# Performance work log

Measured on AMD Instinct MI355X. Metric: run time of the kernel, lower is better.

## Reference

```python
import jax, jax.numpy as jnp
import numpy as np
import math

B, N, C, H = 4, 4096, 1024, 4
D = C // H            # per-head channel dim = 256
KV_SIZE = 1024        # config.KV_sizec, used as the score scale
EPS = 1e-5            # InstanceNorm2d default eps


def setup_inputs() -> dict:
    key = jax.random.key(0)
    ks = jax.random.split(key, 9)
    f = lambda k, shape: jax.random.normal(k, shape, dtype=jnp.float32) * 0.05
    return {
        'S':   f(ks[0], (B, N, C)),
        'SKV': f(ks[1], (B, N, C)),
        'T':   f(ks[2], (B, N, C)),
        'TKV': f(ks[3], (B, N, C)),
        'Wq':  f(ks[4], (H, D, D)),   # per-head torch Linear weights [out,in]
        'Wk':  f(ks[5], (H, D, D)),
        'Wv':  f(ks[6], (H, D, D)),
        'Wout':  f(ks[7], (C, C)),
        'Woutd': f(ks[8], (C, C)),
    }


def _heads(x, W):
    # x: [B,N,C] split into H chunks of D along channels; per-head Linear (no bias).
    xh = x.reshape(B, N, H, D)
    return jnp.einsum('bnhd,hed->bhne', xh, W)  # [B,H,N,D]


def _inorm(s):
    # InstanceNorm2d (affine=False): normalize over the last two dims per (batch, head).
    m = jnp.mean(s, axis=(-2, -1), keepdims=True)
    v = jnp.var(s, axis=(-2, -1), keepdims=True)
    return (s - m) * jax.lax.rsqrt(v + EPS)


def _attend(Q, K, V, Wout):
    # Channel attention: scores [B,H,D,D], sequence dim contracted.
    scores = jnp.einsum('bhni,bhnj->bhij', Q, K) / math.sqrt(KV_SIZE)
    probs = jax.nn.softmax(_inorm(scores), axis=-1)
    ctx = jnp.einsum('bhij,bhnj->bhin', probs, V)          # [B,H,D,N]
    # permute(0,3,2,1) -> [B,N,D,H], then view merges (D,H) with head fastest.
    ctx = jnp.transpose(ctx, (0, 3, 2, 1)).reshape(B, N, C)
    return jnp.einsum('bnc,oc->bno', ctx, Wout)


def reference(S, SKV, T, TKV, Wq, Wk, Wv, Wout, Woutd):
    Q  = _heads(S,   Wq); K  = _heads(SKV, Wk); V  = _heads(SKV, Wv)
    Qd = _heads(T,   Wq); Kd = _heads(TKV, Wk); Vd = _heads(TKV, Wv)
    S2T   = _attend(Q,  Kd, Vd, Wout)   # cross: S queries, T keys/values
    T2S   = _attend(Qd, K,  V,  Woutd)  # cross: T queries, S keys/values
    S_out = _attend(Q,  K,  V,  Wout)   # self on S
    T_out = _attend(Qd, Kd, Vd, Woutd)  # self on T
    return (S_out, T2S, S2T, T_out)
```

## Files before the change

### kernel.cpp

```cpp
#include <hip/hip_runtime.h>
#include <hip/hip_bf16.h>
#include <cstdint>

using bf16 = __hip_bfloat16;
typedef __attribute__((ext_vector_type(8))) short bf16x8v;
typedef __attribute__((ext_vector_type(4))) float f32x4v;

__device__ __forceinline__ void gload_lds16(const void* g, void* l) {
  __builtin_amdgcn_global_load_lds(
      (const __attribute__((address_space(1))) void*)g,
      (__attribute__((address_space(3))) void*)l, 16, 0, 0);
}

__device__ __forceinline__ unsigned short f2bu(float x) {
  union { __hip_bfloat16 h; unsigned short u; } cv;
  cv.h = __float2bfloat16(x);
  return cv.u;
}

__device__ __forceinline__ bf16x8v cvt8(const f32x4v lo, const f32x4v hi) {
  bf16x8v t;
  t[0] = (short)f2bu(lo[0]); t[1] = (short)f2bu(lo[1]);
  t[2] = (short)f2bu(lo[2]); t[3] = (short)f2bu(lo[3]);
  t[4] = (short)f2bu(hi[0]); t[5] = (short)f2bu(hi[1]);
  t[6] = (short)f2bu(hi[2]); t[7] = (short)f2bu(hi[3]);
  return t;
}

struct GemmP {
  const void* A; const void* B; const void* A2; const void* B2; void* C;
  int K, lda, ldb, ldc, tilesN, swz;
  int d0, d1, d2;
  long long sA0, sA1, sA2, sA3;
  long long sB0, sB1, sB2, sB3;
  long long sC0, sC1, sC2, sC3;
  long long zA, zB, zC;
  float scale;
};

template<int OUT_F32, int AF32, int BF32>
__global__ __launch_bounds__(256, 4)
void gemm_bt(GemmP p)
{
  constexpr int EA = AF32 ? 4 : 2;
  constexpr int EB = BF32 ? 4 : 2;
  constexpr int ABYTES = 128 * 64 * EA;
  constexpr int BBYTES = 128 * 64 * EB;
  constexpr int SEGA = ABYTES / 4096;
  constexpr int SEGB = BBYTES / 4096;
  __shared__ __attribute__((aligned(1024))) char smem[ABYTES + BBYTES];
  const int tid  = threadIdx.x;
  const int lane = tid & 63;
  const int wid  = tid >> 6;

  int bx = blockIdx.x;
  if (p.swz) {
    const int nx = gridDim.x;
    const int q = nx >> 3, r = nx & 7;
    const int xcd = bx & 7, loc = bx >> 3;
    bx = (xcd < r ? xcd * (q + 1) : r * (q + 1) + (xcd - r) * q) + loc;
  }
  const int tn = bx % p.tilesN;
  const int tm = bx / p.tilesN;
  int idx = blockIdx.y;
  const int i0 = idx % p.d0; idx /= p.d0;
  const int i1 = idx % p.d1; idx /= p.d1;
  const int i2 = idx % p.d2;
  const int i3 = idx / p.d2;

  const char* Abase = (const char*)((p.A2 && i2) ? p.A2 : p.A);
  const char* Bbase = (const char*)((p.B2 && i2) ? p.B2 : p.B);
  const long long offA = (long long)i0*p.sA0 + (long long)i1*p.sA1 +
                         (long long)i2*p.sA2 + (long long)i3*p.sA3 +
                         (long long)blockIdx.z*p.zA;
  const long long offB = (long long)i0*p.sB0 + (long long)i1*p.sB1 +
                         (long long)i2*p.sB2 + (long long)i3*p.sB3 +
                         (long long)blockIdx.z*p.zB;
  const char* Am = Abase + offA * EA;
  const char* Bm = Bbase + offB * EB;
  const int bm = tm * 128, bn = tn * 128;

  const char* asrc[SEGA]; int aseg[SEGA];
  #pragma unroll
  for (int r = 0; r < SEGA; ++r) {
    const int oseg = (wid * SEGA + r) * 1024;
    const int o = oseg + lane * 16;
    int row, srcoff;
    if constexpr (AF32) { row = o >> 8; const int s = (o >> 4) & 15; srcoff = (s ^ (row & 15)) * 4; }
    else               { row = o >> 7; const int s = (o >> 4) & 7;  srcoff = (s ^ (row & 7)) * 8;  }
    aseg[r] = oseg;
    asrc[r] = Am + ((long long)(bm + row) * p.lda + srcoff) * EA;
  }
  const char* bsrc[SEGB]; int bseg[SEGB];
  #pragma unroll
  for (int r = 0; r < SEGB; ++r) {
    const int oseg = (wid * SEGB + r) * 1024;
    const int o = oseg + lane * 16;
    int row, srcoff;
    if constexpr (BF32) { row = o >> 8; const int s = (o >> 4) & 15; srcoff = (s ^ (row & 15)) * 4; }
    else               { row = o >> 7; const int s = (o >> 4) & 7;  srcoff = (s ^ (row & 7)) * 8;  }
    bseg[r] = oseg;
    bsrc[r] = Bm + ((long long)(bn + row) * p.ldb + srcoff) * EB;
  }

  f32x4v acc[4][4];
  #pragma unroll
  for (int i = 0; i < 4; ++i)
    #pragma unroll
    for (int j = 0; j < 4; ++j) acc[i][j] = (f32x4v){0.f, 0.f, 0.f, 0.f};

  const int wr = wid >> 1, wc = wid & 1;
  const int fr_a = wr * 64 + (lane & 15);
  const int fr_b = wc * 64 + (lane & 15);
  const int fch  = lane >> 4;

  const int nK = p.K / 64;
  for (int kt = 0; kt < nK; ++kt) {
    #pragma unroll
    for (int r = 0; r < SEGA; ++r) { gload_lds16(asrc[r], smem + aseg[r]); asrc[r] += 64 * EA; }
    #pragma unroll
    for (int r = 0; r < SEGB; ++r) { gload_lds16(bsrc[r], smem + ABYTES + bseg[r]); bsrc[r] += 64 * EB; }
    __syncthreads();
    #pragma unroll
    for (int kk = 0; kk < 2; ++kk) {
      bf16x8v a[4], b[4];
      #pragma unroll
      for (int mi = 0; mi < 4; ++mi) {
        const int row = fr_a + mi * 16;
        if constexpr (AF32) {
          const int c2 = (fch + kk * 4) * 2;
          const f32x4v lo = *(const f32x4v*)(smem + row * 256 + ((c2 ^ (row & 15)) << 4));
          const f32x4v hi = *(const f32x4v*)(smem + row * 256 + (((c2 + 1) ^ (row & 15)) << 4));
          a[mi] = cvt8(lo, hi);
        } else {
          a[mi] = *(const bf16x8v*)(smem + row * 128 + (((fch + kk * 4) ^ (row & 7)) << 4));
        }
      }
      #pragma unroll
      for (int ni = 0; ni < 4; ++ni) {
        const int row = fr_b + ni * 16;
        if constexpr (BF32) {
          const int c2 = (fch + kk * 4) * 2;
          const f32x4v lo = *(const f32x4v*)(smem + ABYTES + row * 256 + ((c2 ^ (row & 15)) << 4));
          const f32x4v hi = *(const f32x4v*)(smem + ABYTES + row * 256 + (((c2 + 1) ^ (row & 15)) << 4));
          b[ni] = cvt8(lo, hi);
        } else {
          b[ni] = *(const bf16x8v*)(smem + ABYTES + row * 128 + (((fch + kk * 4) ^ (row & 7)) << 4));
        }
      }
      #pragma unroll
      for (int mi = 0; mi < 4; ++mi)
        #pragma unroll
        for (int ni = 0; ni < 4; ++ni)
          acc[mi][ni] = __builtin_amdgcn_mfma_f32_16x16x32_bf16(a[mi], b[ni], acc[mi][ni], 0, 0, 0);
    }
    __syncthreads();
  }

  const long long coff = (long long)i0*p.sC0 + (long long)i1*p.sC1 +
                         (long long)i2*p.sC2 + (long long)i3*p.sC3 +
                         (long long)blockIdx.z*p.zC;
  const int col0 = bn + wc * 64 + (lane & 15);
  const int row0 = bm + wr * 64 + ((lane >> 4) << 2);
  if (OUT_F32) {
    float* Cp = (float*)p.C + coff;
    #pragma unroll
    for (int mi = 0; mi < 4; ++mi)
      #pragma unroll
      for (int ni = 0; ni < 4; ++ni)
        #pragma unroll
        for (int j = 0; j < 4; ++j)
          Cp[(size_t)(row0 + mi*16 + j) * p.ldc + (col0 + ni*16)] = acc[mi][ni][j] * p.scale;
  } else {
    bf16* Cp = (bf16*)p.C + coff;
    #pragma unroll
    for (int mi = 0; mi < 4; ++mi)
      #pragma unroll
      for (int ni = 0; ni < 4; ++ni)
        #pragma unroll
        for (int j = 0; j < 4; ++j)
          Cp[(size_t)(row0 + mi*16 + j) * p.ldc + (col0 + ni*16)] =
              __float2bfloat16(acc[mi][ni][j] * p.scale);
  }
}

struct KVP {
  const float* X0; const float* X1;
  const bf16* Wk; const bf16* Wv;
  bf16* KT; bf16* Vc;
};

__global__ __launch_bounds__(256, 2)
void kv_fused(KVP p)
{
  __shared__ __attribute__((aligned(1024))) char smem[65536];
  const int tid = threadIdx.x, lane = tid & 63, wid = tid >> 6;
  const int jt = blockIdx.x & 1, nt = blockIdx.x >> 1;
  int idx = blockIdx.y;
  const int h = idx & 3; idx >>= 2;
  const int b = idx & 3; idx >>= 2;
  const int vi = idx;
  const float* X = (vi ? p.X1 : p.X0) + (size_t)b * 4194304 + (size_t)h * 256;
  const bf16* Wk = p.Wk + (size_t)h * 65536;
  const bf16* Wv = p.Wv + (size_t)h * 65536;
  const int n0 = nt * 128, j0 = jt * 128;

  const float* xsrc[8];
  #pragma unroll
  for (int r = 0; r < 8; ++r) {
    const int o = (wid * 8 + r) * 1024 + lane * 16;
    const int row = o >> 8, s = (o >> 4) & 15;
    xsrc[r] = X + (size_t)(n0 + row) * 1024 + (s ^ (row & 15)) * 4;
  }
  const bf16 *wksrc[4], *wvsrc[4];
  #pragma unroll
  for (int r = 0; r < 4; ++r) {
    const int o = (wid * 4 + r) * 1024 + lane * 16;
    const int row = o >> 7, s = (o >> 4) & 7;
    wksrc[r] = Wk + (size_t)(j0 + row) * 256 + (s ^ (row & 7)) * 8;
    wvsrc[r] = Wv + (size_t)(j0 + row) * 256 + (s ^ (row & 7)) * 8;
  }

  f32x4v accK[4][4], accV[4][4];
  #pragma unroll
  for (int i = 0; i < 4; ++i)
    #pragma unroll
    for (int j = 0; j < 4; ++j) {
      accK[i][j] = (f32x4v){0.f, 0.f, 0.f, 0.f};
      accV[i][j] = (f32x4v){0.f, 0.f, 0.f, 0.f};
    }

  const int wr = wid >> 1, wc = wid & 1;
  const int frW = wr * 64 + (lane & 15);
  const int frX = wc * 64 + (lane & 15);
  const int fch = lane >> 4;

  for (int kt = 0; kt < 4; ++kt) {
    #pragma unroll
    for (int r = 0; r < 8; ++r) { gload_lds16(xsrc[r], smem + (wid * 8 + r) * 1024); xsrc[r] += 64; }
    #pragma unroll
    for (int r = 0; r < 4; ++r) {
      gload_lds16(wksrc[r], smem + 32768 + (wid * 4 + r) * 1024); wksrc[r] += 64;
      gload_lds16(wvsrc[r], smem + 49152 + (wid * 4 + r) * 1024); wvsrc[r] += 64;
    }
    __syncthreads();
    #pragma unroll
    for (int kk = 0; kk < 2; ++kk) {
      bf16x8v wk[4], wv[4], x[4];
      #pragma unroll
      for (int mi = 0; mi < 4; ++mi) {
        const int row = frW + mi * 16;
        const int byo = row * 128 + (((fch + kk * 4) ^ (row & 7)) << 4);
        wk[mi] = *(const bf16x8v*)(smem + 32768 + byo);
        wv[mi] = *(const bf16x8v*)(smem + 49152 + byo);
      }
      #pragma unroll
      for (int ni = 0; ni < 4; ++ni) {
        const int row = frX + ni * 16;
        const int c2 = (fch + kk * 4) * 2;
        const f32x4v lo = *(const f32x4v*)(smem + row * 256 + ((c2 ^ (row & 15)) << 4));
        const f32x4v hi = *(const f32x4v*)(smem + row * 256 + (((c2 + 1) ^ (row & 15)) << 4));
        x[ni] = cvt8(lo, hi);
      }
      #pragma unroll
      for (int mi = 0; mi < 4; ++mi)
        #pragma unroll
        for (int ni = 0; ni < 4; ++ni) {
          accK[mi][ni] = __builtin_amdgcn_mfma_f32_16x16x32_bf16(wk[mi], x[ni], accK[mi][ni], 0, 0, 0);
          accV[ni][mi] = __builtin_amdgcn_mfma_f32_16x16x32_bf16(x[ni], wv[mi], accV[ni][mi], 0, 0, 0);
        }
    }
    __syncthreads();
  }

  const size_t kbase = (size_t)vi * 16777216 + (size_t)b * 4194304 + (size_t)h * 1048576;
  const size_t vbase = (size_t)vi * 16777216 + (size_t)b * 4194304;
  bf16* Kp = p.KT + kbase;
  bf16* Vp = p.Vc + vbase;
  const int rW = ((lane >> 4) << 2);
  #pragma unroll
  for (int mi = 0; mi < 4; ++mi)
    #pragma unroll
    for (int ni = 0; ni < 4; ++ni)
      #pragma unroll
      for (int j = 0; j < 4; ++j) {
        const int jrow = j0 + wr * 64 + mi * 16 + rW + j;
        const int ncol = n0 + wc * 64 + ni * 16 + (lane & 15);
        Kp[(size_t)jrow * 4096 + ncol] = __float2bfloat16(accK[mi][ni][j]);
        const int nrow = n0 + wc * 64 + ni * 16 + rW + j;
        const int jcol = j0 + wr * 64 + mi * 16 + (lane & 15);
        Vp[(size_t)nrow * 1024 + h * 256 + jcol] = __float2bfloat16(accV[ni][mi][j]);
      }
}

__global__ void cvt3_f32_bf16(const float* __restrict__ a0, const float* __restrict__ a1,
                              const float* __restrict__ a2,
                              unsigned short* __restrict__ out, long long ostride, int n4) {
  const int i = blockIdx.x * 256 + threadIdx.x;
  if (i >= n4) return;
  const float* src = (blockIdx.y == 0) ? a0 : (blockIdx.y == 1) ? a1 : a2;
  const float4 v = ((const float4*)src)[i];
  ushort4 o;
  o.x = f2bu(v.x); o.y = f2bu(v.y); o.z = f2bu(v.z); o.w = f2bu(v.w);
  ((ushort4*)(out + (size_t)blockIdx.y * ostride))[i] = o;
}

__global__ void wpre_kernel(const float* __restrict__ Wout, const float* __restrict__ Woutd,
                            bf16* __restrict__ Wpre) {
  const int w = blockIdx.y;
  const int flat = blockIdx.x * 256 + threadIdx.x;
  const float* Wsrc = w ? Woutd : Wout;
  const int o  = flat >> 10;
  const int c2 = flat & 1023;
  const int h  = c2 >> 8;
  const int i  = c2 & 255;
  Wpre[(size_t)w * 1048576 + flat] = __float2bfloat16(Wsrc[o * 1024 + i * 4 + h]);
}

__global__ __launch_bounds__(256)
void stats_quarter(const float* __restrict__ sp, float* __restrict__ st) {
  const int m = blockIdx.x >> 2, q = blockIdx.x & 3;
  const size_t PS = 4194304;
  const float* s = sp + (size_t)m * 65536 + (size_t)q * 16384;
  const int tid = threadIdx.x, lane = tid & 63, w = tid >> 6;

  float sum = 0.f, sq = 0.f;
  for (int i = tid; i < 4096; i += 256) {
    const float4 a = ((const float4*)s)[i];
    const float4 b = ((const float4*)(s + PS))[i];
    const float4 c = ((const float4*)(s + 2 * PS))[i];
    const float4 d = ((const float4*)(s + 3 * PS))[i];
    const float x0 = (a.x + b.x) + (c.x + d.x);
    const float x1 = (a.y + b.y) + (c.y + d.y);
    const float x2 = (a.z + b.z) + (c.z + d.z);
    const float x3 = (a.w + b.w) + (c.w + d.w);
    sum += (x0 + x1) + (x2 + x3);
    sq  += (x0 * x0 + x1 * x1) + (x2 * x2 + x3 * x3);
  }
  #pragma unroll
  for (int o = 32; o; o >>= 1) { sum += __shfl_xor(sum, o); sq += __shfl_xor(sq, o); }
  __shared__ float red[8];
  if (lane == 0) { red[w] = sum; red[4 + w] = sq; }
  __syncthreads();
  if (tid == 0) {
    st[blockIdx.x * 2]     = (red[0] + red[1]) + (red[2] + red[3]);
    st[blockIdx.x * 2 + 1] = (red[4] + red[5]) + (red[6] + red[7]);
  }
}

__global__ __launch_bounds__(256)
void softmax_t(const float* __restrict__ sp, const float* __restrict__ st,
               bf16* __restrict__ pr) {
  const int m = blockIdx.x >> 2, iq = blockIdx.x & 3;
  const size_t PS = 4194304;
  const float sum = (st[m*8+0] + st[m*8+2]) + (st[m*8+4] + st[m*8+6]);
  const float sq  = (st[m*8+1] + st[m*8+3]) + (st[m*8+5] + st[m*8+7]);
  const float mean = sum * (1.f / 65536.f);
  const float var  = sq * (1.f / 65536.f) - mean * mean;
  const float inv  = rsqrtf(var + 1e-5f);

  const int tid = threadIdx.x;
  const int i  = iq * 64 + (tid & 63);
  const int jq = tid >> 6;
  const float* cb = sp + (size_t)m * 65536 + i;

  float e[64];
  float se = 0.f;
  #pragma unroll
  for (int jj = 0; jj < 64; ++jj) {
    const size_t o = (size_t)(jq * 64 + jj) * 256;
    const float v = (cb[o] + cb[PS + o]) + (cb[2 * PS + o] + cb[3 * PS + o]);
    e[jj] = __expf((v - mean) * inv);
    se += e[jj];
  }
  __shared__ float seb[256];
  seb[tid] = se;
  __syncthreads();
  const int c = tid & 63;
  const float rvs = 1.f / ((seb[c] + seb[c + 64]) + (seb[c + 128] + seb[c + 192]));
  bf16* pc = pr + (size_t)m * 65536 + i;
  #pragma unroll
  for (int jj = 0; jj < 64; ++jj)
    pc[(size_t)(jq * 64 + jj) * 256] = __float2bfloat16(e[jj] * rvs);
}

extern "C" void kernel_launch(void* const* d_in, const int* in_sizes, int n_in,
                              void* d_out, int out_size, void* d_ws, size_t ws_size,
                              hipStream_t stream)
{
  const float* S     = (const float*)d_in[0];
  const float* SKV   = (const float*)d_in[1];
  const float* T     = (const float*)d_in[2];
  const float* TKV   = (const float*)d_in[3];
  const float* Wq    = (const float*)d_in[4];
  const float* Wk    = (const float*)d_in[5];
  const float* Wv    = (const float*)d_in[6];
  const float* Wout  = (const float*)d_in[7];
  const float* Woutd = (const float*)d_in[8];
  float* out = (float*)d_out;

  const int Hd = 4, Dd = 256;
  const long long NC  = 4096ll * 1024;
  const long long BNC = 4 * NC;
  const long long HDN = 1048576;

  char* ws = (char*)d_ws;
  size_t off = 0;
  auto alloc = [&](size_t bytes) -> void* {
    void* pp = ws + off; off += (bytes + 255) & ~(size_t)255; return pp;
  };
  bf16*  Wqb    = (bf16*)alloc((size_t)Hd * Dd * Dd * 2);
  bf16*  Wkb    = (bf16*)alloc((size_t)Hd * Dd * Dd * 2);
  bf16*  Wvb    = (bf16*)alloc((size_t)Hd * Dd * Dd * 2);
  bf16*  Wpre   = (bf16*)alloc(2ull * 1024 * 1024 * 2);
  bf16*  QT     = (bf16*)alloc(2 * BNC * 2);
  bf16*  KT     = (bf16*)alloc(2 * BNC * 2);
  bf16*  Vc     = (bf16*)alloc(2 * BNC * 2);
  float* sparts = (float*)alloc(4ull * 4194304 * 4);
  float* stats  = (float*)alloc(256ull * 2 * 4);
  bf16*  probsT = (bf16*)alloc(64ull * 65536 * 2);
  bf16*  Weff   = QT;
  if (ws_size < off) return;

  {
    const int w4 = (Hd * Dd * Dd) / 4;
    cvt3_f32_bf16<<<dim3((w4 + 255) / 256, 3), dim3(256), 0, stream>>>(
        Wq, Wk, Wv, (unsigned short*)Wqb, (long long)Hd * Dd * Dd, w4);
    wpre_kernel<<<dim3(4096, 2), dim3(256), 0, stream>>>(Wout, Woutd, Wpre);
  }

  GemmP g{};

  g.A = Wqb; g.B = S; g.A2 = nullptr; g.B2 = T; g.C = QT;
  g.K = 256; g.lda = 256; g.ldb = 1024; g.ldc = 4096; g.tilesN = 32; g.swz = 0;
  g.d0 = 4; g.d1 = 4; g.d2 = 2;
  g.sA0 = 65536; g.sA1 = 0;  g.sA2 = 0;   g.sA3 = 0;
  g.sB0 = 256;   g.sB1 = NC; g.sB2 = 0;   g.sB3 = 0;
  g.sC0 = HDN;   g.sC1 = NC; g.sC2 = BNC; g.sC3 = 0;
  g.zA = 0; g.zB = 0; g.zC = 0;
  g.scale = 1.f;
  gemm_bt<0, 0, 1><<<dim3(2 * 32, 32), dim3(256), 0, stream>>>(g);

  {
    KVP kv{SKV, TKV, Wkb, Wvb, KT, Vc};
    kv_fused<<<dim3(64, 32), dim3(256), 0, stream>>>(kv);
  }

  g.A = KT; g.B = QT; g.A2 = nullptr; g.B2 = nullptr; g.C = sparts;
  g.K = 1024; g.lda = 4096; g.ldb = 4096; g.ldc = 256; g.tilesN = 2; g.swz = 0;
  g.d0 = 4; g.d1 = 4; g.d2 = 2;
  g.sA0 = HDN;   g.sA1 = NC;     g.sA2 = BNC;     g.sA3 = 0;
  g.sB0 = HDN;   g.sB1 = NC;     g.sB2 = 0;       g.sB3 = BNC;
  g.sC0 = 65536; g.sC1 = 262144; g.sC2 = 1048576; g.sC3 = 2097152;
  g.zA = 1024; g.zB = 1024; g.zC = 4194304;
  g.scale = 0.03125f;
  gemm_bt<1, 0, 0><<<dim3(2 * 2, 64, 4), dim3(256), 0, stream>>>(g);

  stats_quarter<<<dim3(256), dim3(256), 0, stream>>>(sparts, stats);
  softmax_t<<<dim3(256), dim3(256), 0, stream>>>(sparts, stats, probsT);

  g.A = Wpre; g.B = probsT; g.C = Weff;
  g.K = 256; g.lda = 1024; g.ldb = 256; g.ldc = 1024; g.tilesN = 2; g.swz = 0;
  g.d0 = 4; g.d1 = 4; g.d2 = 2;
  g.sA0 = 256;   g.sA1 = 0;       g.sA2 = 0;       g.sA3 = 1048576;
  g.sB0 = 65536; g.sB1 = 262144;  g.sB2 = 1048576; g.sB3 = 2097152;
  g.sC0 = 256;   g.sC1 = 1048576; g.sC2 = 4194304; g.sC3 = 8388608;
  g.zA = 0; g.zB = 0; g.zC = 0;
  g.scale = 1.f;
  gemm_bt<0, 0, 0><<<dim3(8 * 2, 64), dim3(256), 0, stream>>>(g);

  g.A = Vc; g.B = Weff; g.C = out;
  g.K = 1024; g.lda = 1024; g.ldb = 1024; g.ldc = 1024; g.tilesN = 8; g.swz = 1;
  g.d0 = 4; g.d1 = 2; g.d2 = 2;
  g.sA0 = NC;      g.sA1 = BNC;     g.sA2 = 0;       g.sA3 = 0;
  g.sB0 = 1048576; g.sB1 = 4194304; g.sB2 = 8388608; g.sB3 = 0;
  g.sC0 = NC;      g.sC1 = 2 * BNC; g.sC2 = BNC;     g.sC3 = 0;
  g.scale = 1.f;
  gemm_bt<1, 0, 0><<<dim3(32 * 8, 16), dim3(256), 0, stream>>>(g);

  (void)in_sizes; (void)n_in; (void)out_size;
}
```

Measured before the change: 445.3 us.

## Add 256x256-tile 512-thread GEMM kernel for score and output GEMMs

Adds a new bf16 MFMA GEMM kernel with 256x256 output tiles, 8 waves, 128KB double-buffered LDS and direct global-to-LDS loads. It is used for the split-K score GEMM and the final Vc x Weff output GEMM in place of the 128x128 kernel. The larger tiles raise arithmetic intensity and reduce global/L2 traffic per FLOP. The trade-off is far fewer blocks (e.g. 256 for the score GEMM), higher register pressure from 32 accumulators per thread, and heavy LDS use that limits occupancy.

```diff
diff --git a/kernel.cpp b/kernel.cpp
--- a/kernel.cpp
+++ b/kernel.cpp
@@ -175,6 +175,154 @@
     bf16* Cp = (bf16*)p.C + coff;
     #pragma unroll
     for (int mi = 0; mi < 4; ++mi)
+      #pragma unroll
+      for (int ni = 0; ni < 4; ++ni)
+        #pragma unroll
+        for (int j = 0; j < 4; ++j)
+          Cp[(size_t)(row0 + mi*16 + j) * p.ldc + (col0 + ni*16)] =
+              __float2bfloat16(acc[mi][ni][j] * p.scale);
+  }
+}
+
+struct G256P {
+  const bf16* A; const bf16* B; void* C;
+  int lda, ldb, ldc, nt, tilesN, swz;
+  int d0, d1, d2;
+  long long sA0, sA1, sA2, sA3;
+  long long sB0, sB1, sB2, sB3;
+  long long sC0, sC1, sC2, sC3;
+  long long zA, zB, zC;
+  float scale;
+};
+
+template<int OUT_F32>
+__global__ __launch_bounds__(512, 2)
+void gemm256_bt(G256P p)
+{
+  __shared__ __attribute__((aligned(1024))) char smem[131072];
+  const int tid = threadIdx.x, lane = tid & 63, wid = tid >> 6;
+
+  int bx = blockIdx.x;
+  if (p.swz) {
+    const int nx = gridDim.x;
+    const int q = nx >> 3, r = nx & 7;
+    const int xcd = bx & 7, loc = bx >> 3;
+    bx = (xcd < r ? xcd * (q + 1) : r * (q + 1) + (xcd - r) * q) + loc;
+  }
+  const int tn = bx % p.tilesN, tm = bx / p.tilesN;
+  int idx = blockIdx.y;
+  const int i0 = idx % p.d0; idx /= p.d0;
+  const int i1 = idx % p.d1; idx /= p.d1;
+  const int i2 = idx % p.d2;
+  const int i3 = idx / p.d2;
+
+  const bf16* Am = p.A + ((long long)i0*p.sA0 + (long long)i1*p.sA1 +
+                          (long long)i2*p.sA2 + (long long)i3*p.sA3 +
+                          (long long)blockIdx.z*p.zA) + (long long)tm * 256 * p.lda;
+  const bf16* Bm = p.B + ((long long)i0*p.sB0 + (long long)i1*p.sB1 +
+                          (long long)i2*p.sB2 + (long long)i3*p.sB3 +
+                          (long long)blockIdx.z*p.zB) + (long long)tn * 256 * p.ldb;
+
+  const bf16 *asrc[4], *bsrc[4]; int seg[4];
+  #pragma unroll
+  for (int r = 0; r < 4; ++r) {
+    const int oseg = (wid * 4 + r) * 1024;
+    const int o = oseg + lane * 16;
+    const int row = o >> 7;
+    const int ch  = ((o >> 4) & 7) ^ (row & 7);
+    seg[r] = oseg;
+    asrc[r] = Am + (long long)row * p.lda + ch * 8;
+    bsrc[r] = Bm + (long long)row * p.ldb + ch * 8;
+  }
+
+  #pragma unroll
+  for (int r = 0; r < 4; ++r) {
+    gload_lds16(asrc[r], smem + seg[r]);
+    gload_lds16(bsrc[r], smem + 32768 + seg[r]);
+    asrc[r] += 64; bsrc[r] += 64;
+  }
+
+  f32x4v acc[8][4];
+  #pragma unroll
+  for (int i = 0; i < 8; ++i)
+    #pragma unroll
+    for (int j = 0; j < 4; ++j) acc[i][j] = (f32x4v){0.f, 0.f, 0.f, 0.f};
+
+  const int wr = wid >> 2, wc = wid & 3;
+  const int rA = wr * 128 + (lane & 15);
+  const int rB = wc * 64 + (lane & 15);
+  const int fch = lane >> 4;
+
+  for (int t = 0; t < p.nt; ++t) {
+    const int cb = (t & 1) << 16;
+    if (t + 1 < p.nt) {
+      const int nb = ((t + 1) & 1) << 16;
+      #pragma unroll
+      for (int r = 0; r < 4; ++r) {
+        gload_lds16(asrc[r], smem + nb + seg[r]);
+        gload_lds16(bsrc[r], smem + nb + 32768 + seg[r]);
+        asrc[r] += 64; bsrc[r] += 64;
+      }
+      asm volatile("s_waitcnt vmcnt(8)" ::: "memory");
+    } else {
+      asm volatile("s_waitcnt vmcnt(0)" ::: "memory");
+    }
+    __builtin_amdgcn_s_barrier();
+    __builtin_amdgcn_sched_barrier(0);
+
+    bf16x8v bfr[2][4];
+    #pragma unroll
+    for (int kk = 0; kk < 2; ++kk)
+      #pragma unroll
+      for (int ni = 0; ni < 4; ++ni) {
+        const int row = rB + ni * 16;
+        bfr[kk][ni] = *(const bf16x8v*)(smem + cb + 32768 + row * 128 +
+                                        (((fch + kk * 4) ^ (row & 7)) << 4));
+      }
+    #pragma unroll
+    for (int q = 0; q < 4; ++q) {
+      bf16x8v afr[2][2];
+      #pragma unroll
+      for (int kk = 0; kk < 2; ++kk)
+        #pragma unroll
+        for (int mi = 0; mi < 2; ++mi) {
+          const int row = rA + (q * 2 + mi) * 16;
+          afr[kk][mi] = *(const bf16x8v*)(smem + cb + row * 128 +
+                                          (((fch + kk * 4) ^ (row & 7)) << 4));
+        }
+      __builtin_amdgcn_s_setprio(1);
+      #pragma unroll
+      for (int kk = 0; kk < 2; ++kk)
+        #pragma unroll
+        for (int mi = 0; mi < 2; ++mi)
+          #pragma unroll
+          for (int ni = 0; ni < 4; ++ni)
+            acc[q * 2 + mi][ni] = __builtin_amdgcn_mfma_f32_16x16x32_bf16(
+                afr[kk][mi], bfr[kk][ni], acc[q * 2 + mi][ni], 0, 0, 0);
+      __builtin_amdgcn_s_setprio(0);
+    }
+    __builtin_amdgcn_sched_barrier(0);
+    __builtin_amdgcn_s_barrier();
+  }
+
+  const long long coff = (long long)i0*p.sC0 + (long long)i1*p.sC1 +
+                         (long long)i2*p.sC2 + (long long)i3*p.sC3 +
+                         (long long)blockIdx.z*p.zC;
+  const int col0 = tn * 256 + wc * 64 + (lane & 15);
+  const int row0 = tm * 256 + wr * 128 + ((lane >> 4) << 2);
+  if (OUT_F32) {
+    float* Cp = (float*)p.C + coff;
+    #pragma unroll
+    for (int mi = 0; mi < 8; ++mi)
+      #pragma unroll
+      for (int ni = 0; ni < 4; ++ni)
+        #pragma unroll
+        for (int j = 0; j < 4; ++j)
+          Cp[(size_t)(row0 + mi*16 + j) * p.ldc + (col0 + ni*16)] = acc[mi][ni][j] * p.scale;
+  } else {
+    bf16* Cp = (bf16*)p.C + coff;
+    #pragma unroll
+    for (int mi = 0; mi < 8; ++mi)
       #pragma unroll
       for (int ni = 0; ni < 4; ++ni)
         #pragma unroll
@@ -446,20 +594,22 @@
     kv_fused<<<dim3(64, 32), dim3(256), 0, stream>>>(kv);
   }
 
-  g.A = KT; g.B = QT; g.A2 = nullptr; g.B2 = nullptr; g.C = sparts;
-  g.K = 1024; g.lda = 4096; g.ldb = 4096; g.ldc = 256; g.tilesN = 2; g.swz = 0;
-  g.d0 = 4; g.d1 = 4; g.d2 = 2;
-  g.sA0 = HDN;   g.sA1 = NC;     g.sA2 = BNC;     g.sA3 = 0;
-  g.sB0 = HDN;   g.sB1 = NC;     g.sB2 = 0;       g.sB3 = BNC;
-  g.sC0 = 65536; g.sC1 = 262144; g.sC2 = 1048576; g.sC3 = 2097152;
-  g.zA = 1024; g.zB = 1024; g.zC = 4194304;
-  g.scale = 0.03125f;
-  gemm_bt<1, 0, 0><<<dim3(2 * 2, 64, 4), dim3(256), 0, stream>>>(g);
+  G256P h{};
+
+  h.A = KT; h.B = QT; h.C = sparts;
+  h.lda = 4096; h.ldb = 4096; h.ldc = 256; h.nt = 16; h.tilesN = 1; h.swz = 0;
+  h.d0 = 4; h.d1 = 4; h.d2 = 2;
+  h.sA0 = HDN;   h.sA1 = NC;     h.sA2 = BNC;     h.sA3 = 0;
+  h.sB0 = HDN;   h.sB1 = NC;     h.sB2 = 0;       h.sB3 = BNC;
+  h.sC0 = 65536; h.sC1 = 262144; h.sC2 = 1048576; h.sC3 = 2097152;
+  h.zA = 1024; h.zB = 1024; h.zC = 4194304;
+  h.scale = 0.03125f;
+  gemm256_bt<1><<<dim3(1, 64, 4), dim3(512), 0, stream>>>(h);
 
   stats_quarter<<<dim3(256), dim3(256), 0, stream>>>(sparts, stats);
   softmax_t<<<dim3(256), dim3(256), 0, stream>>>(sparts, stats, probsT);
 
-  g.A = Wpre; g.B = probsT; g.C = Weff;
+  g.A = Wpre; g.B = probsT; g.A2 = nullptr; g.B2 = nullptr; g.C = Weff;
   g.K = 256; g.lda = 1024; g.ldb = 256; g.ldc = 1024; g.tilesN = 2; g.swz = 0;
   g.d0 = 4; g.d1 = 4; g.d2 = 2;
   g.sA0 = 256;   g.sA1 = 0;       g.sA2 = 0;       g.sA3 = 1048576;
@@ -469,14 +619,15 @@
   g.scale = 1.f;
   gemm_bt<0, 0, 0><<<dim3(8 * 2, 64), dim3(256), 0, stream>>>(g);
 
-  g.A = Vc; g.B = Weff; g.C = out;
-  g.K = 1024; g.lda = 1024; g.ldb = 1024; g.ldc = 1024; g.tilesN = 8; g.swz = 1;
-  g.d0 = 4; g.d1 = 2; g.d2 = 2;
-  g.sA0 = NC;      g.sA1 = BNC;     g.sA2 = 0;       g.sA3 = 0;
-  g.sB0 = 1048576; g.sB1 = 4194304; g.sB2 = 8388608; g.sB3 = 0;
-  g.sC0 = NC;      g.sC1 = 2 * BNC; g.sC2 = BNC;     g.sC3 = 0;
-  g.scale = 1.f;
-  gemm_bt<1, 0, 0><<<dim3(32 * 8, 16), dim3(256), 0, stream>>>(g);
+  h.A = Vc; h.B = Weff; h.C = out;
+  h.lda = 1024; h.ldb = 1024; h.ldc = 1024; h.nt = 16; h.tilesN = 4; h.swz = 1;
+  h.d0 = 4; h.d1 = 2; h.d2 = 2;
+  h.sA0 = NC;      h.sA1 = BNC;     h.sA2 = 0;       h.sA3 = 0;
+  h.sB0 = 1048576; h.sB1 = 4194304; h.sB2 = 8388608; h.sB3 = 0;
+  h.sC0 = NC;      h.sC1 = 2 * BNC; h.sC2 = BNC;     h.sC3 = 0;
+  h.zA = 0; h.zB = 0; h.zC = 0;
+  h.scale = 1.f;
+  gemm256_bt<1><<<dim3(16 * 4, 16), dim3(512), 0, stream>>>(h);
 
   (void)in_sizes; (void)n_in; (void)out_size;
 }
```

Result: no change. 450.0 us (+1.0%).
